# Kernel optimization log

Measured on AMD Instinct MI355X. Metric: run time of the kernel, lower is better.

The kernel has to match this reference:

```python
import jax, jax.numpy as jnp
import numpy as np

B, T, D, H, E = 4, 2048, 1024, 2048, 8

def setup_inputs() -> dict:
    key = jax.random.key(0)
    ks = jax.random.split(key, 7)
    s_in = 1.0 / np.sqrt(D)
    s_hid = 1.0 / np.sqrt(H)
    return {
        "x": jax.random.normal(ks[0], (B, T, D), dtype=jnp.float32),
        "Wg": jax.random.uniform(ks[1], (D, E), jnp.float32, -s_in, s_in),
        "bg": jax.random.uniform(ks[2], (E,), jnp.float32, -s_in, s_in),
        "W1": jax.random.uniform(ks[3], (E, D, H), jnp.float32, -s_in, s_in),
        "b1": jax.random.uniform(ks[4], (E, H), jnp.float32, -s_in, s_in),
        "W2": jax.random.uniform(ks[5], (E, H, D), jnp.float32, -s_hid, s_hid),
        "b2": jax.random.uniform(ks[6], (E, D), jnp.float32, -s_hid, s_hid),
    }

def reference(x, Wg, bg, W1, b1, W2, b2):
    # gating: [B,T,E]
    gate = jax.nn.softmax(jnp.einsum('btd,de->bte', x, Wg) + bg, axis=-1)
    # all experts densely: hidden [B,T,E,H]
    h = jax.nn.relu(jnp.einsum('btd,edh->bteh', x, W1) + b1)
    # expert outputs [B,T,E,D]
    eo = jnp.einsum('bteh,ehd->bted', h, W2) + b2
    # softmax-weighted sum over experts -> [B,T,D]
    return jnp.einsum('bte,bted->btd', gate, eo)
```

## Files before the change

### kernel.cpp

```cpp
#include <hip/hip_runtime.h>
#include <hip/hip_bf16.h>
#include <stdint.h>


typedef __bf16 bf16_t;
typedef bf16_t bf16x8 __attribute__((ext_vector_type(8)));
typedef bf16_t bf16x4 __attribute__((ext_vector_type(4)));
typedef float  f32x4  __attribute__((ext_vector_type(4)));

#define Ddim 1024
#define Hdim 2048
#define Edim 8
#define Mdim 8192

__device__ __forceinline__ void async16(const void* g, const void* l) {
  __builtin_amdgcn_global_load_lds(
      (const __attribute__((address_space(1))) void*)(uintptr_t)g,
      (__attribute__((address_space(3))) void*)(uint32_t)(uintptr_t)l,
      16, 0, 0);
}

#define MFMA(a, b, c) __builtin_amdgcn_mfma_f32_16x16x32_bf16((a), (b), (c), 0, 0, 0)

#define WAIT_LGKM0() do {                                  \
    asm volatile("s_waitcnt lgkmcnt(0)" ::: "memory");     \
    __builtin_amdgcn_sched_barrier(0);                     \
  } while (0)
#define WAIT_VM(n) do {                                    \
    asm volatile("s_waitcnt vmcnt(" #n ")" ::: "memory");  \
    __builtin_amdgcn_sched_barrier(0);                     \
  } while (0)

__global__ void gating_kernel(const float* __restrict__ x,
                              const float* __restrict__ Wg,
                              const float* __restrict__ bg,
                              float* __restrict__ gate) {
  const int lane = threadIdx.x & 63;
  const int wid  = threadIdx.x >> 6;
  const int t    = blockIdx.x * 4 + wid;
  const float* xr = x + (size_t)t * Ddim;
  float acc[8] = {0.f,0.f,0.f,0.f,0.f,0.f,0.f,0.f};
  for (int i = lane; i < Ddim; i += 64) {
    float xv = xr[i];
    f32x4 a = *(const f32x4*)(Wg + (size_t)i * 8);
    f32x4 b = *(const f32x4*)(Wg + (size_t)i * 8 + 4);
    acc[0] += xv * a[0]; acc[1] += xv * a[1];
    acc[2] += xv * a[2]; acc[3] += xv * a[3];
    acc[4] += xv * b[0]; acc[5] += xv * b[1];
    acc[6] += xv * b[2]; acc[7] += xv * b[3];
  }
  #pragma unroll
  for (int e = 0; e < 8; ++e) {
    #pragma unroll
    for (int off = 32; off; off >>= 1)
      acc[e] += __shfl_xor(acc[e], off, 64);
  }
  if (lane == 0) {
    float l[8], mx = -1e30f;
    #pragma unroll
    for (int e = 0; e < 8; ++e) { l[e] = acc[e] + bg[e]; mx = fmaxf(mx, l[e]); }
    float s = 0.f;
    #pragma unroll
    for (int e = 0; e < 8; ++e) { l[e] = __expf(l[e] - mx); s += l[e]; }
    float inv = 1.f / s;
    #pragma unroll
    for (int e = 0; e < 8; ++e) gate[(size_t)t * 8 + e] = l[e] * inv;
  }
}

__global__ void cvt_x(const float* __restrict__ a, bf16_t* __restrict__ o) {
  const size_t i = ((size_t)blockIdx.x * 256 + threadIdx.x) * 8;
  f32x4 v0 = *(const f32x4*)(a + i);
  f32x4 v1 = *(const f32x4*)(a + i + 4);
  bf16x8 b;
  b[0]=(bf16_t)v0[0]; b[1]=(bf16_t)v0[1]; b[2]=(bf16_t)v0[2]; b[3]=(bf16_t)v0[3];
  b[4]=(bf16_t)v1[0]; b[5]=(bf16_t)v1[1]; b[6]=(bf16_t)v1[2]; b[7]=(bf16_t)v1[3];
  *(bf16x8*)(o + i) = b;
}

__global__ void transpose_f32_bf16(const float* __restrict__ src,
                                   bf16_t* __restrict__ dst, int R, int C) {
  __shared__ bf16_t tile[32][33];
  const size_t zo = (size_t)blockIdx.z * (size_t)R * C;
  src += zo; dst += zo;
  const int r0 = blockIdx.y * 32, c0 = blockIdx.x * 32;
  const int tr = threadIdx.x >> 3;
  const int tc = (threadIdx.x & 7) * 4;
  f32x4 v = *(const f32x4*)(src + (size_t)(r0 + tr) * C + c0 + tc);
  tile[tr][tc+0] = (bf16_t)v[0]; tile[tr][tc+1] = (bf16_t)v[1];
  tile[tr][tc+2] = (bf16_t)v[2]; tile[tr][tc+3] = (bf16_t)v[3];
  __syncthreads();
  bf16x4 o;
  o[0] = tile[tc+0][tr]; o[1] = tile[tc+1][tr];
  o[2] = tile[tc+2][tr]; o[3] = tile[tc+3][tr];
  *(bf16x4*)(dst + (size_t)(c0 + tr) * R + r0 + tc) = o;
}

__launch_bounds__(512, 2)
__global__ void gemm1_kernel(const bf16_t* __restrict__ A,
                             const bf16_t* __restrict__ W1tAll,
                             const float*  __restrict__ gate,
                             const float*  __restrict__ b1,
                             bf16_t* __restrict__ hgAll,
                             int e0) {
  __shared__ alignas(16) bf16_t sA[2][256 * 64];
  __shared__ alignas(16) bf16_t sB[2][256 * 64];

  const int tid  = threadIdx.x;
  const int lane = tid & 63;
  const int wid  = tid >> 6;
  const int wm   = wid >> 2, wn = wid & 3;
  const int lrow = lane & 15, quad = lane >> 4;
  const int sb   = quad ^ (lrow & 7);

  const int z = blockIdx.z;
  const int e = e0 + z;
  const bf16_t* Bt = W1tAll + (size_t)z * Hdim * Ddim;
  bf16_t* hg = hgAll + (size_t)z * (size_t)Mdim * Hdim;
  const float* bias = b1 + (size_t)e * Hdim;

  const int bid = blockIdx.y * 8 + blockIdx.x;
  const int xcd = bid & 7, loc = bid >> 3;
  const int tileM = (xcd * 4 + (loc >> 3)) * 256;
  const int tileN = (loc & 7) * 256;

  const int trow = tid >> 3;
  const int tsw  = ((tid & 7) ^ (trow & 7)) << 4;
  const int ldst = tid << 4;
  const size_t SA = (size_t)64 * Ddim * 2;

  const char* a0 = (const char*)(A  + (size_t)(tileM + trow) * Ddim) + tsw;
  const char* b0 = (const char*)(Bt + (size_t)(tileN + trow) * Ddim) + tsw;
  char* curA = (char*)&sA[0][0]; char* nxtA = (char*)&sA[1][0];
  char* curB = (char*)&sB[0][0]; char* nxtB = (char*)&sB[1][0];

  async16(a0,          curA + 0 * 8192 + ldst);
  async16(a0 + 2 * SA, curA + 2 * 8192 + ldst);
  async16(b0,          curB + 0 * 8192 + ldst);
  async16(b0 + SA,     curB + 1 * 8192 + ldst);
  async16(b0 + 2 * SA, curB + 2 * 8192 + ldst);
  async16(b0 + 3 * SA, curB + 3 * 8192 + ldst);
  async16(a0 + SA,     curA + 1 * 8192 + ldst);
  async16(a0 + 3 * SA, curA + 3 * 8192 + ldst);
  a0 += 128; b0 += 128;
  WAIT_VM(0);
  __builtin_amdgcn_s_barrier();

  f32x4 acc[8][4] = {};
  const int offA0 = (wm * 128 + lrow) * 128 + sb * 16;
  const int offA1 = (wm * 128 + lrow) * 128 + (sb ^ 4) * 16;
  const int offB0 = (wn * 64  + lrow) * 128 + sb * 16;
  const int offB1 = (wn * 64  + lrow) * 128 + (sb ^ 4) * 16;

  #pragma unroll 1
  for (int kk = 0; kk < Ddim / 64; ++kk) {
    const bool notlast = (kk + 1 < Ddim / 64);
    bf16x8 afr[4][2], bfr[4][2];

    #pragma unroll
    for (int i = 0; i < 4; ++i) {
      afr[i][0] = *(const bf16x8*)(curA + offA0 + i * 2048);
      afr[i][1] = *(const bf16x8*)(curA + offA1 + i * 2048);
    }
    #pragma unroll
    for (int j = 0; j < 2; ++j) {
      bfr[j][0] = *(const bf16x8*)(curB + offB0 + j * 2048);
      bfr[j][1] = *(const bf16x8*)(curB + offB1 + j * 2048);
    }
    if (notlast) {
      async16(a0,          nxtA + 0 * 8192 + ldst);
      async16(a0 + 2 * SA, nxtA + 2 * 8192 + ldst);
    }
    __builtin_amdgcn_s_barrier();
    WAIT_LGKM0();
    __builtin_amdgcn_s_setprio(1);
    #pragma unroll
    for (int i = 0; i < 4; ++i)
      #pragma unroll
      for (int j = 0; j < 2; ++j) {
        acc[i][j] = MFMA(afr[i][0], bfr[j][0], acc[i][j]);
        acc[i][j] = MFMA(afr[i][1], bfr[j][1], acc[i][j]);
      }
    __builtin_amdgcn_s_setprio(0);
    __builtin_amdgcn_s_barrier();

    #pragma unroll
    for (int j = 0; j < 2; ++j) {
      bfr[2 + j][0] = *(const bf16x8*)(curB + offB0 + (2 + j) * 2048);
      bfr[2 + j][1] = *(const bf16x8*)(curB + offB1 + (2 + j) * 2048);
    }
    if (notlast) {
      async16(b0,          nxtB + 0 * 8192 + ldst);
      async16(b0 + SA,     nxtB + 1 * 8192 + ldst);
      async16(b0 + 2 * SA, nxtB + 2 * 8192 + ldst);
      async16(b0 + 3 * SA, nxtB + 3 * 8192 + ldst);
    }
    __builtin_amdgcn_s_barrier();
    WAIT_LGKM0();
    __builtin_amdgcn_s_setprio(1);
    #pragma unroll
    for (int i = 0; i < 4; ++i)
      #pragma unroll
      for (int j = 0; j < 2; ++j) {
        acc[i][2 + j] = MFMA(afr[i][0], bfr[2 + j][0], acc[i][2 + j]);
        acc[i][2 + j] = MFMA(afr[i][1], bfr[2 + j][1], acc[i][2 + j]);
      }
    __builtin_amdgcn_s_setprio(0);
    if (notlast) { WAIT_VM(6); } else { WAIT_VM(0); }
    __builtin_amdgcn_s_barrier();

    #pragma unroll
    for (int i = 0; i < 4; ++i) {
      afr[i][0] = *(const bf16x8*)(curA + offA0 + 8192 + i * 2048);
      afr[i][1] = *(const bf16x8*)(curA + offA1 + 8192 + i * 2048);
    }
    if (notlast) {
      async16(a0 + SA,     nxtA + 1 * 8192 + ldst);
      async16(a0 + 3 * SA, nxtA + 3 * 8192 + ldst);
    }
    __builtin_amdgcn_s_barrier();
    WAIT_LGKM0();
    __builtin_amdgcn_s_setprio(1);
    #pragma unroll
    for (int i = 0; i < 4; ++i)
      #pragma unroll
      for (int j = 0; j < 2; ++j) {
        acc[4 + i][j] = MFMA(afr[i][0], bfr[j][0], acc[4 + i][j]);
        acc[4 + i][j] = MFMA(afr[i][1], bfr[j][1], acc[4 + i][j]);
      }
    __builtin_amdgcn_s_setprio(0);
    __builtin_amdgcn_s_barrier();

    __builtin_amdgcn_s_setprio(1);
    #pragma unroll
    for (int i = 0; i < 4; ++i)
      #pragma unroll
      for (int j = 0; j < 2; ++j) {
        acc[4 + i][2 + j] = MFMA(afr[i][0], bfr[2 + j][0], acc[4 + i][2 + j]);
        acc[4 + i][2 + j] = MFMA(afr[i][1], bfr[2 + j][1], acc[4 + i][2 + j]);
      }
    __builtin_amdgcn_s_setprio(0);
    if (notlast) { WAIT_VM(2); } else { WAIT_VM(0); }
    __builtin_amdgcn_s_barrier();

    a0 += 128; b0 += 128;
    char* t;
    t = curA; curA = nxtA; nxtA = t;
    t = curB; curB = nxtB; nxtB = t;
  }

  const int col0 = tileN + wn * 64 + lrow;
  float bcol[4];
  #pragma unroll
  for (int j = 0; j < 4; ++j) bcol[j] = bias[col0 + j * 16];
  #pragma unroll
  for (int i = 0; i < 8; ++i) {
    #pragma unroll
    for (int r = 0; r < 4; ++r) {
      const int row = tileM + wm * 128 + i * 16 + quad * 4 + r;
      const float g = gate[(size_t)row * 8 + e];
      #pragma unroll
      for (int j = 0; j < 4; ++j) {
        float v = acc[i][j][r] + bcol[j];
        v = fmaxf(v, 0.f) * g;
        hg[(size_t)row * Hdim + col0 + j * 16] = (bf16_t)v;
      }
    }
  }
}

template <int G, bool FIRST>
__launch_bounds__(512, 2)
__global__ void gemm2_kernel(const bf16_t* __restrict__ hgAll,
                             const bf16_t* __restrict__ W2tAll,
                             const float*  __restrict__ gate,
                             const float*  __restrict__ b2,
                             float* __restrict__ out,
                             int e0) {
  __shared__ alignas(16) bf16_t sA[2][256 * 64];
  __shared__ alignas(16) bf16_t sB[2][128 * 64];

  const int tid  = threadIdx.x;
  const int lane = tid & 63;
  const int wid  = tid >> 6;
  const int wm   = wid >> 2, wn = wid & 3;
  const int lrow = lane & 15, quad = lane >> 4;
  const int sb   = quad ^ (lrow & 7);

  const int bid = blockIdx.y * 8 + blockIdx.x;
  const int xcd = bid & 7, loc = bid >> 3;
  const int tileM = (xcd * 4 + (loc >> 3)) * 256;
  const int tileN = (loc & 7) * 128;

  const int trow = tid >> 3;
  const int tsw  = ((tid & 7) ^ (trow & 7)) << 4;
  const int ldst = tid << 4;
  const size_t S = (size_t)64 * Hdim * 2;

  const char* a0 = (const char*)(hgAll  + (size_t)(tileM + trow) * Hdim) + tsw;
  const char* b0 = (const char*)(W2tAll + (size_t)(tileN + trow) * Hdim) + tsw;
  char* curA = (char*)&sA[0][0]; char* nxtA = (char*)&sA[1][0];
  char* curB = (char*)&sB[0][0]; char* nxtB = (char*)&sB[1][0];

  async16(a0,         curA + 0 * 8192 + ldst);
  async16(a0 + 2 * S, curA + 2 * 8192 + ldst);
  async16(b0,         curB + 0 * 8192 + ldst);
  async16(b0 + S,     curB + 1 * 8192 + ldst);
  async16(a0 + S,     curA + 1 * 8192 + ldst);
  async16(a0 + 3 * S, curA + 3 * 8192 + ldst);
  a0 += 128; b0 += 128;
  WAIT_VM(0);
  __builtin_amdgcn_s_barrier();

  f32x4 acc[8][2] = {};
  const int offA0 = (wm * 128 + lrow) * 128 + sb * 16;
  const int offA1 = (wm * 128 + lrow) * 128 + (sb ^ 4) * 16;
  const int offB0 = (wn * 32  + lrow) * 128 + sb * 16;
  const int offB1 = (wn * 32  + lrow) * 128 + (sb ^ 4) * 16;

  const int NKT = G * (Hdim / 64);
  #pragma unroll 1
  for (int kk = 0; kk < NKT; ++kk) {
    const bool notlast = (kk + 1 < NKT);
    if (notlast && (((kk + 1) & 31) == 0)) {
      const int gn = (kk + 1) >> 5;
      a0 = (const char*)(hgAll  + (size_t)gn * Mdim * Hdim
                         + (size_t)(tileM + trow) * Hdim) + tsw;
      b0 = (const char*)(W2tAll + (size_t)gn * Ddim * Hdim
                         + (size_t)(tileN + trow) * Hdim) + tsw;
    }
    bf16x8 afr[4][2], bfr[2][2];

    #pragma unroll
    for (int i = 0; i < 4; ++i) {
      afr[i][0] = *(const bf16x8*)(curA + offA0 + i * 2048);
      afr[i][1] = *(const bf16x8*)(curA + offA1 + i * 2048);
    }
    #pragma unroll
    for (int j = 0; j < 2; ++j) {
      bfr[j][0] = *(const bf16x8*)(curB + offB0 + j * 2048);
      bfr[j][1] = *(const bf16x8*)(curB + offB1 + j * 2048);
    }
    if (notlast) {
      async16(a0,         nxtA + 0 * 8192 + ldst);
      async16(a0 + 2 * S, nxtA + 2 * 8192 + ldst);
      async16(b0,         nxtB + 0 * 8192 + ldst);
      async16(b0 + S,     nxtB + 1 * 8192 + ldst);
    }
    __builtin_amdgcn_s_barrier();
    WAIT_LGKM0();
    __builtin_amdgcn_s_setprio(1);
    #pragma unroll
    for (int i = 0; i < 4; ++i)
      #pragma unroll
      for (int j = 0; j < 2; ++j) {
        acc[i][j] = MFMA(afr[i][0], bfr[j][0], acc[i][j]);
        acc[i][j] = MFMA(afr[i][1], bfr[j][1], acc[i][j]);
      }
    __builtin_amdgcn_s_setprio(0);
    if (notlast) { WAIT_VM(4); } else { WAIT_VM(0); }
    __builtin_amdgcn_s_barrier();

    #pragma unroll
    for (int i = 0; i < 4; ++i) {
      afr[i][0] = *(const bf16x8*)(curA + offA0 + 8192 + i * 2048);
      afr[i][1] = *(const bf16x8*)(curA + offA1 + 8192 + i * 2048);
    }
    if (notlast) {
      async16(a0 + S,     nxtA + 1 * 8192 + ldst);
      async16(a0 + 3 * S, nxtA + 3 * 8192 + ldst);
    }
    __builtin_amdgcn_s_barrier();
    WAIT_LGKM0();
    __builtin_amdgcn_s_setprio(1);
    #pragma unroll
    for (int i = 0; i < 4; ++i)
      #pragma unroll
      for (int j = 0; j < 2; ++j) {
        acc[4 + i][j] = MFMA(afr[i][0], bfr[j][0], acc[4 + i][j]);
        acc[4 + i][j] = MFMA(afr[i][1], bfr[j][1], acc[4 + i][j]);
      }
    __builtin_amdgcn_s_setprio(0);
    if (notlast) { WAIT_VM(2); } else { WAIT_VM(0); }
    __builtin_amdgcn_s_barrier();

    a0 += 128; b0 += 128;
    char* t;
    t = curA; curA = nxtA; nxtA = t;
    t = curB; curB = nxtB; nxtB = t;
  }

  const int col0 = tileN + wn * 32 + lrow;
  float b2c[2][G];
  #pragma unroll
  for (int j = 0; j < 2; ++j)
    #pragma unroll
    for (int g = 0; g < G; ++g)
      b2c[j][g] = b2[(size_t)(e0 + g) * Ddim + col0 + j * 16];

  #pragma unroll
  for (int i = 0; i < 8; ++i) {
    #pragma unroll
    for (int r = 0; r < 4; ++r) {
      const int row = tileM + wm * 128 + i * 16 + quad * 4 + r;
      const float* gr = gate + (size_t)row * 8 + e0;
      float gv[G];
      #pragma unroll
      for (int g = 0; g < G; ++g) gv[g] = gr[g];
      #pragma unroll
      for (int j = 0; j < 2; ++j) {
        float v = acc[i][j][r];
        #pragma unroll
        for (int g = 0; g < G; ++g) v += gv[g] * b2c[j][g];
        if (FIRST) out[(size_t)row * Ddim + col0 + j * 16] = v;
        else       out[(size_t)row * Ddim + col0 + j * 16] += v;
      }
    }
  }
}

extern "C" void kernel_launch(void* const* d_in, const int* in_sizes, int n_in,
                              void* d_out, int out_size, void* d_ws, size_t ws_size,
                              hipStream_t stream) {
  const float* x  = (const float*)d_in[0];
  const float* Wg = (const float*)d_in[1];
  const float* bg = (const float*)d_in[2];
  const float* W1 = (const float*)d_in[3];
  const float* b1 = (const float*)d_in[4];
  const float* W2 = (const float*)d_in[5];
  const float* b2 = (const float*)d_in[6];
  float* out = (float*)d_out;

  int G = 1;
  if      (ws_size >= (size_t)(17 + 40 * 8) << 20) G = 8;
  else if (ws_size >= (size_t)(17 + 40 * 4) << 20) G = 4;
  else if (ws_size >= (size_t)(17 + 40 * 2) << 20) G = 2;

  char* ws = (char*)d_ws;
  float*  gate = (float*)ws;
  bf16_t* xb   = (bf16_t*)(ws + (1u << 20));
  bf16_t* W1t  = (bf16_t*)(ws + (17u << 20));
  bf16_t* W2t  = (bf16_t*)(ws + ((size_t)(17 + 4 * G) << 20));
  bf16_t* hg   = (bf16_t*)(ws + ((size_t)(17 + 8 * G) << 20));

  gating_kernel<<<Mdim / 4, 256, 0, stream>>>(x, Wg, bg, gate);
  cvt_x<<<(Mdim * Ddim) / (256 * 8), 256, 0, stream>>>(x, xb);

  const int nGroups = Edim / G;
  for (int gi = 0; gi < nGroups; ++gi) {
    const int e0 = gi * G;
    transpose_f32_bf16<<<dim3(Hdim / 32, Ddim / 32, G), 256, 0, stream>>>(
        W1 + (size_t)e0 * Ddim * Hdim, W1t, Ddim, Hdim);
    transpose_f32_bf16<<<dim3(Ddim / 32, Hdim / 32, G), 256, 0, stream>>>(
        W2 + (size_t)e0 * Hdim * Ddim, W2t, Hdim, Ddim);

    gemm1_kernel<<<dim3(Hdim / 256, Mdim / 256, G), 512, 0, stream>>>(
        xb, W1t, gate, b1, hg, e0);

    const dim3 g2(Ddim / 128, Mdim / 256);
    const bool first = (gi == 0);
    if (G == 8)      gemm2_kernel<8, true ><<<g2, 512, 0, stream>>>(hg, W2t, gate, b2, out, e0);
    else if (G == 4) {
      if (first)     gemm2_kernel<4, true ><<<g2, 512, 0, stream>>>(hg, W2t, gate, b2, out, e0);
      else           gemm2_kernel<4, false><<<g2, 512, 0, stream>>>(hg, W2t, gate, b2, out, e0);
    } else if (G == 2) {
      if (first)     gemm2_kernel<2, true ><<<g2, 512, 0, stream>>>(hg, W2t, gate, b2, out, e0);
      else           gemm2_kernel<2, false><<<g2, 512, 0, stream>>>(hg, W2t, gate, b2, out, e0);
    } else {
      if (first)     gemm2_kernel<1, true ><<<g2, 512, 0, stream>>>(hg, W2t, gate, b2, out, e0);
      else           gemm2_kernel<1, false><<<g2, 512, 0, stream>>>(hg, W2t, gate, b2, out, e0);
    }
  }
}
```

Measured before the change: 764.7 us.

## Simplify GEMM main loops to single-phase prefetch and reshape gemm2 warp tiling

Both GEMM kernels drop the four-phase interleaved schedule, where LDS reads, async global loads and MFMA blocks alternated with many barriers. They now issue all next-tile async loads at the top of each k-step, read the full fragment set, run every MFMA, and then wait and barrier once. This cuts barriers and waitcnt points per iteration, but holds more fragment registers live and gives up the finer overlap of loads with compute. gemm2's warp layout also moves from a 128x32 to a 64x64 per-warp tile, which balances A and B fragment reuse.

```diff
diff --git a/kernel.cpp b/kernel.cpp
--- a/kernel.cpp
+++ b/kernel.cpp
@@ -22,12 +22,8 @@
 
 #define MFMA(a, b, c) __builtin_amdgcn_mfma_f32_16x16x32_bf16((a), (b), (c), 0, 0, 0)
 
-#define WAIT_LGKM0() do {                                  \
-    asm volatile("s_waitcnt lgkmcnt(0)" ::: "memory");     \
-    __builtin_amdgcn_sched_barrier(0);                     \
-  } while (0)
-#define WAIT_VM(n) do {                                    \
-    asm volatile("s_waitcnt vmcnt(" #n ")" ::: "memory");  \
+#define WAIT_VM0() do {                                    \
+    asm volatile("s_waitcnt vmcnt(0)" ::: "memory");       \
     __builtin_amdgcn_sched_barrier(0);                     \
   } while (0)
 
@@ -135,15 +131,15 @@
   char* curB = (char*)&sB[0][0]; char* nxtB = (char*)&sB[1][0];
 
   async16(a0,          curA + 0 * 8192 + ldst);
+  async16(a0 + SA,     curA + 1 * 8192 + ldst);
   async16(a0 + 2 * SA, curA + 2 * 8192 + ldst);
+  async16(a0 + 3 * SA, curA + 3 * 8192 + ldst);
   async16(b0,          curB + 0 * 8192 + ldst);
   async16(b0 + SA,     curB + 1 * 8192 + ldst);
   async16(b0 + 2 * SA, curB + 2 * 8192 + ldst);
   async16(b0 + 3 * SA, curB + 3 * 8192 + ldst);
-  async16(a0 + SA,     curA + 1 * 8192 + ldst);
-  async16(a0 + 3 * SA, curA + 3 * 8192 + ldst);
   a0 += 128; b0 += 128;
-  WAIT_VM(0);
+  WAIT_VM0();
   __builtin_amdgcn_s_barrier();
 
   f32x4 acc[8][4] = {};
@@ -155,94 +151,39 @@
   #pragma unroll 1
   for (int kk = 0; kk < Ddim / 64; ++kk) {
     const bool notlast = (kk + 1 < Ddim / 64);
-    bf16x8 afr[4][2], bfr[4][2];
-
-    #pragma unroll
-    for (int i = 0; i < 4; ++i) {
+    __builtin_amdgcn_sched_barrier(0);
+    if (notlast) {
+      async16(a0,          nxtA + 0 * 8192 + ldst);
+      async16(a0 + SA,     nxtA + 1 * 8192 + ldst);
+      async16(a0 + 2 * SA, nxtA + 2 * 8192 + ldst);
+      async16(a0 + 3 * SA, nxtA + 3 * 8192 + ldst);
+      async16(b0,          nxtB + 0 * 8192 + ldst);
+      async16(b0 + SA,     nxtB + 1 * 8192 + ldst);
+      async16(b0 + 2 * SA, nxtB + 2 * 8192 + ldst);
+      async16(b0 + 3 * SA, nxtB + 3 * 8192 + ldst);
+    }
+    bf16x8 afr[8][2], bfr[4][2];
+    #pragma unroll
+    for (int i = 0; i < 8; ++i) {
       afr[i][0] = *(const bf16x8*)(curA + offA0 + i * 2048);
       afr[i][1] = *(const bf16x8*)(curA + offA1 + i * 2048);
     }
     #pragma unroll
-    for (int j = 0; j < 2; ++j) {
+    for (int j = 0; j < 4; ++j) {
       bfr[j][0] = *(const bf16x8*)(curB + offB0 + j * 2048);
       bfr[j][1] = *(const bf16x8*)(curB + offB1 + j * 2048);
     }
-    if (notlast) {
-      async16(a0,          nxtA + 0 * 8192 + ldst);
-      async16(a0 + 2 * SA, nxtA + 2 * 8192 + ldst);
-    }
-    __builtin_amdgcn_s_barrier();
-    WAIT_LGKM0();
     __builtin_amdgcn_s_setprio(1);
     #pragma unroll
-    for (int i = 0; i < 4; ++i)
-      #pragma unroll
-      for (int j = 0; j < 2; ++j) {
+    for (int i = 0; i < 8; ++i)
+      #pragma unroll
+      for (int j = 0; j < 4; ++j) {
         acc[i][j] = MFMA(afr[i][0], bfr[j][0], acc[i][j]);
         acc[i][j] = MFMA(afr[i][1], bfr[j][1], acc[i][j]);
       }
     __builtin_amdgcn_s_setprio(0);
+    WAIT_VM0();
     __builtin_amdgcn_s_barrier();
-
-    #pragma unroll
-    for (int j = 0; j < 2; ++j) {
-      bfr[2 + j][0] = *(const bf16x8*)(curB + offB0 + (2 + j) * 2048);
-      bfr[2 + j][1] = *(const bf16x8*)(curB + offB1 + (2 + j) * 2048);
-    }
-    if (notlast) {
-      async16(b0,          nxtB + 0 * 8192 + ldst);
-      async16(b0 + SA,     nxtB + 1 * 8192 + ldst);
-      async16(b0 + 2 * SA, nxtB + 2 * 8192 + ldst);
-      async16(b0 + 3 * SA, nxtB + 3 * 8192 + ldst);
-    }
-    __builtin_amdgcn_s_barrier();
-    WAIT_LGKM0();
-    __builtin_amdgcn_s_setprio(1);
-    #pragma unroll
-    for (int i = 0; i < 4; ++i)
-      #pragma unroll
-      for (int j = 0; j < 2; ++j) {
-        acc[i][2 + j] = MFMA(afr[i][0], bfr[2 + j][0], acc[i][2 + j]);
-        acc[i][2 + j] = MFMA(afr[i][1], bfr[2 + j][1], acc[i][2 + j]);
-      }
-    __builtin_amdgcn_s_setprio(0);
-    if (notlast) { WAIT_VM(6); } else { WAIT_VM(0); }
-    __builtin_amdgcn_s_barrier();
-
-    #pragma unroll
-    for (int i = 0; i < 4; ++i) {
-      afr[i][0] = *(const bf16x8*)(curA + offA0 + 8192 + i * 2048);
-      afr[i][1] = *(const bf16x8*)(curA + offA1 + 8192 + i * 2048);
-    }
-    if (notlast) {
-      async16(a0 + SA,     nxtA + 1 * 8192 + ldst);
-      async16(a0 + 3 * SA, nxtA + 3 * 8192 + ldst);
-    }
-    __builtin_amdgcn_s_barrier();
-    WAIT_LGKM0();
-    __builtin_amdgcn_s_setprio(1);
-    #pragma unroll
-    for (int i = 0; i < 4; ++i)
-      #pragma unroll
-      for (int j = 0; j < 2; ++j) {
-        acc[4 + i][j] = MFMA(afr[i][0], bfr[j][0], acc[4 + i][j]);
-        acc[4 + i][j] = MFMA(afr[i][1], bfr[j][1], acc[4 + i][j]);
-      }
-    __builtin_amdgcn_s_setprio(0);
-    __builtin_amdgcn_s_barrier();
-
-    __builtin_amdgcn_s_setprio(1);
-    #pragma unroll
-    for (int i = 0; i < 4; ++i)
-      #pragma unroll
-      for (int j = 0; j < 2; ++j) {
-        acc[4 + i][2 + j] = MFMA(afr[i][0], bfr[2 + j][0], acc[4 + i][2 + j]);
-        acc[4 + i][2 + j] = MFMA(afr[i][1], bfr[2 + j][1], acc[4 + i][2 + j]);
-      }
-    __builtin_amdgcn_s_setprio(0);
-    if (notlast) { WAIT_VM(2); } else { WAIT_VM(0); }
-    __builtin_amdgcn_s_barrier();
-
     a0 += 128; b0 += 128;
     char* t;
     t = curA; curA = nxtA; nxtA = t;
@@ -283,7 +224,7 @@
   const int tid  = threadIdx.x;
   const int lane = tid & 63;
   const int wid  = tid >> 6;
-  const int wm   = wid >> 2, wn = wid & 3;
+  const int wm   = wid >> 1, wn = wid & 1;
   const int lrow = lane & 15, quad = lane >> 4;
   const int sb   = quad ^ (lrow & 7);
 
@@ -303,25 +244,26 @@
   char* curB = (char*)&sB[0][0]; char* nxtB = (char*)&sB[1][0];
 
   async16(a0,         curA + 0 * 8192 + ldst);
+  async16(a0 + S,     curA + 1 * 8192 + ldst);
   async16(a0 + 2 * S, curA + 2 * 8192 + ldst);
+  async16(a0 + 3 * S, curA + 3 * 8192 + ldst);
   async16(b0,         curB + 0 * 8192 + ldst);
   async16(b0 + S,     curB + 1 * 8192 + ldst);
-  async16(a0 + S,     curA + 1 * 8192 + ldst);
-  async16(a0 + 3 * S, curA + 3 * 8192 + ldst);
   a0 += 128; b0 += 128;
-  WAIT_VM(0);
+  WAIT_VM0();
   __builtin_amdgcn_s_barrier();
 
-  f32x4 acc[8][2] = {};
-  const int offA0 = (wm * 128 + lrow) * 128 + sb * 16;
-  const int offA1 = (wm * 128 + lrow) * 128 + (sb ^ 4) * 16;
-  const int offB0 = (wn * 32  + lrow) * 128 + sb * 16;
-  const int offB1 = (wn * 32  + lrow) * 128 + (sb ^ 4) * 16;
+  f32x4 acc[4][4] = {};
+  const int offA0 = (wm * 64 + lrow) * 128 + sb * 16;
+  const int offA1 = (wm * 64 + lrow) * 128 + (sb ^ 4) * 16;
+  const int offB0 = (wn * 64 + lrow) * 128 + sb * 16;
+  const int offB1 = (wn * 64 + lrow) * 128 + (sb ^ 4) * 16;
 
   const int NKT = G * (Hdim / 64);
   #pragma unroll 1
   for (int kk = 0; kk < NKT; ++kk) {
     const bool notlast = (kk + 1 < NKT);
+    __builtin_amdgcn_sched_barrier(0);
     if (notlast && (((kk + 1) & 31) == 0)) {
       const int gn = (kk + 1) >> 5;
       a0 = (const char*)(hgAll  + (size_t)gn * Mdim * Hdim
@@ -329,86 +271,61 @@
       b0 = (const char*)(W2tAll + (size_t)gn * Ddim * Hdim
                          + (size_t)(tileN + trow) * Hdim) + tsw;
     }
-    bf16x8 afr[4][2], bfr[2][2];
-
+    if (notlast) {
+      async16(a0,         nxtA + 0 * 8192 + ldst);
+      async16(a0 + S,     nxtA + 1 * 8192 + ldst);
+      async16(a0 + 2 * S, nxtA + 2 * 8192 + ldst);
+      async16(a0 + 3 * S, nxtA + 3 * 8192 + ldst);
+      async16(b0,         nxtB + 0 * 8192 + ldst);
+      async16(b0 + S,     nxtB + 1 * 8192 + ldst);
+    }
+    bf16x8 afr[4][2], bfr[4][2];
     #pragma unroll
     for (int i = 0; i < 4; ++i) {
       afr[i][0] = *(const bf16x8*)(curA + offA0 + i * 2048);
       afr[i][1] = *(const bf16x8*)(curA + offA1 + i * 2048);
     }
     #pragma unroll
-    for (int j = 0; j < 2; ++j) {
+    for (int j = 0; j < 4; ++j) {
       bfr[j][0] = *(const bf16x8*)(curB + offB0 + j * 2048);
       bfr[j][1] = *(const bf16x8*)(curB + offB1 + j * 2048);
     }
-    if (notlast) {
-      async16(a0,         nxtA + 0 * 8192 + ldst);
-      async16(a0 + 2 * S, nxtA + 2 * 8192 + ldst);
-      async16(b0,         nxtB + 0 * 8192 + ldst);
-      async16(b0 + S,     nxtB + 1 * 8192 + ldst);
-    }
-    __builtin_amdgcn_s_barrier();
-    WAIT_LGKM0();
     __builtin_amdgcn_s_setprio(1);
     #pragma unroll
     for (int i = 0; i < 4; ++i)
       #pragma unroll
-      for (int j = 0; j < 2; ++j) {
+      for (int j = 0; j < 4; ++j) {
         acc[i][j] = MFMA(afr[i][0], bfr[j][0], acc[i][j]);
         acc[i][j] = MFMA(afr[i][1], bfr[j][1], acc[i][j]);
       }
     __builtin_amdgcn_s_setprio(0);
-    if (notlast) { WAIT_VM(4); } else { WAIT_VM(0); }
+    WAIT_VM0();
     __builtin_amdgcn_s_barrier();
-
-    #pragma unroll
-    for (int i = 0; i < 4; ++i) {
-      afr[i][0] = *(const bf16x8*)(curA + offA0 + 8192 + i * 2048);
-      afr[i][1] = *(const bf16x8*)(curA + offA1 + 8192 + i * 2048);
-    }
-    if (notlast) {
-      async16(a0 + S,     nxtA + 1 * 8192 + ldst);
-      async16(a0 + 3 * S, nxtA + 3 * 8192 + ldst);
-    }
-    __builtin_amdgcn_s_barrier();
-    WAIT_LGKM0();
-    __builtin_amdgcn_s_setprio(1);
-    #pragma unroll
-    for (int i = 0; i < 4; ++i)
-      #pragma unroll
-      for (int j = 0; j < 2; ++j) {
-        acc[4 + i][j] = MFMA(afr[i][0], bfr[j][0], acc[4 + i][j]);
-        acc[4 + i][j] = MFMA(afr[i][1], bfr[j][1], acc[4 + i][j]);
-      }
-    __builtin_amdgcn_s_setprio(0);
-    if (notlast) { WAIT_VM(2); } else { WAIT_VM(0); }
-    __builtin_amdgcn_s_barrier();
-
     a0 += 128; b0 += 128;
     char* t;
     t = curA; curA = nxtA; nxtA = t;
     t = curB; curB = nxtB; nxtB = t;
   }
 
-  const int col0 = tileN + wn * 32 + lrow;
-  float b2c[2][G];
-  #pragma unroll
-  for (int j = 0; j < 2; ++j)
+  const int col0 = tileN + wn * 64 + lrow;
+  float b2c[4][G];
+  #pragma unroll
+  for (int j = 0; j < 4; ++j)
     #pragma unroll
     for (int g = 0; g < G; ++g)
       b2c[j][g] = b2[(size_t)(e0 + g) * Ddim + col0 + j * 16];
 
   #pragma unroll
-  for (int i = 0; i < 8; ++i) {
+  for (int i = 0; i < 4; ++i) {
     #pragma unroll
     for (int r = 0; r < 4; ++r) {
-      const int row = tileM + wm * 128 + i * 16 + quad * 4 + r;
+      const int row = tileM + wm * 64 + i * 16 + quad * 4 + r;
       const float* gr = gate + (size_t)row * 8 + e0;
       float gv[G];
       #pragma unroll
       for (int g = 0; g < G; ++g) gv[g] = gr[g];
       #pragma unroll
-      for (int j = 0; j < 2; ++j) {
+      for (int j = 0; j < 4; ++j) {
         float v = acc[i][j][r];
         #pragma unroll
         for (int g = 0; g < G; ++g) v += gv[g] * b2c[j][g];
```

After: 720.8 us. 1.06x faster.
